# Kernel optimization log

Hardware: AMD Instinct MI355X
Metric: run time of the kernel (lower is better)

## Reference

```python
import jax, jax.numpy as jnp
import numpy as np
import math

B = 4096
D = 768
HID = 256
C_OLD = 100
C_NEW = 100
NUM_CLASSES = 200
EPSILON = 0.05
TAU = 0.1
EPS = 1e-8
NEG_INF = -1e9


def _l2_normalize(x):
    # matches F.normalize(p=2, dim=1, eps=1e-12)
    n = jnp.linalg.norm(x, axis=1, keepdims=True)
    return x / jnp.maximum(n, 1e-12)


def setup_inputs() -> dict:
    key = jax.random.key(0)
    k1, k2, k3, k4, k5, k6, k7 = jax.random.split(key, 7)
    z_u = jax.random.normal(k1, (B, D), dtype=jnp.float32)
    logits = jax.random.normal(k2, (B, NUM_CLASSES), dtype=jnp.float32)
    old_class_indices = jnp.arange(C_OLD, dtype=jnp.int64 if jax.config.jax_enable_x64 else jnp.int32)
    new_class_indices = jnp.arange(C_OLD, C_OLD + C_NEW, dtype=old_class_indices.dtype)
    base_features = jax.random.normal(k3, (B, D), dtype=jnp.float32)
    s = 1.0 / math.sqrt(D)
    f1_w = jax.random.uniform(k4, (HID, D), dtype=jnp.float32, minval=-s, maxval=s)
    f1_b = jax.random.uniform(k5, (HID,), dtype=jnp.float32, minval=-s, maxval=s)
    f2_w = jax.random.uniform(k6, (HID, D), dtype=jnp.float32, minval=-s, maxval=s)
    f2_b = jax.random.uniform(k7, (HID,), dtype=jnp.float32, minval=-s, maxval=s)
    return {"z_u": z_u, "logits": logits, "old_class_indices": old_class_indices,
            "new_class_indices": new_class_indices, "base_features": base_features,
            "f1_w": f1_w, "f1_b": f1_b, "f2_w": f2_w, "f2_b": f2_b}


def reference(z_u, logits, old_class_indices, new_class_indices, base_features,
              f1_w, f1_b, f2_w, f2_b):
    num_old = old_class_indices.shape[0]
    active = jnp.concatenate([old_class_indices, new_class_indices])

    # ---- soft entropy regularization ----
    probs = jax.nn.softmax(logits[:, active], axis=1)   # (B, C_old+C_new)
    mean_probs = probs.mean(axis=0)
    p_old = mean_probs[:num_old].sum()
    p_new = mean_probs[num_old:].sum()
    loss_inter = (p_old * jnp.log(p_old + EPS) + p_new * jnp.log(p_new + EPS)
                  + math.log(2.0))
    p_old_in = mean_probs[:num_old] / (p_old + EPS)
    loss_old_in = jnp.sum(p_old_in * jnp.log(p_old_in + EPS)) + math.log(num_old)
    p_new_in = mean_probs[num_old:] / (p_new + EPS)
    num_new = new_class_indices.shape[0]
    if num_new > 1:
        loss_new_in = jnp.sum(p_new_in * jnp.log(p_new_in + EPS)) + math.log(num_new)
    else:
        loss_new_in = jnp.float32(0.0)
    loss_entropy = loss_inter + loss_old_in + loss_new_in

    # ---- neighborhood mask from frozen base features ----
    base_norm = _l2_normalize(base_features)
    base_sim = base_norm @ base_norm.T                  # (B, B)
    eye = jnp.eye(base_sim.shape[0], dtype=bool)
    mask = (base_sim > EPSILON) & ~eye                  # (B, B) bool

    # ---- contrastive similarities ----
    z_norm = _l2_normalize(z_u)
    sim = z_norm @ z_norm.T                             # (B, B)

    f1_z = z_u @ f1_w.T + f1_b                          # (B, HID)
    f2_z = z_u @ f2_w.T + f2_b
    attn_logits = jnp.where(mask, f1_z @ f2_z.T, NEG_INF)
    w_ik = jax.nn.softmax(attn_logits, axis=1) * mask.astype(sim.dtype)

    exp_sim = jnp.where(eye, 0.0, jnp.exp(sim / TAU))
    denom = exp_sim.sum(axis=1, keepdims=True)
    log_prob = sim / TAU - jnp.log(denom + EPS)

    num_neighbors = mask.sum(axis=1).astype(sim.dtype)  # (B,)
    valid = num_neighbors > 0
    loss_i = -(w_ik * mask.astype(sim.dtype) * log_prob).sum(axis=1)
    per_sample = jnp.where(valid, loss_i / jnp.maximum(num_neighbors, 1.0), 0.0)
    n_valid = valid.sum().astype(sim.dtype)
    loss_contrastive = jnp.where(n_valid > 0,
                                 per_sample.sum() / jnp.maximum(n_valid, 1.0),
                                 0.0)

    total_loss = loss_entropy + loss_contrastive
    return total_loss
```

## Files before the change

### kernel.cpp

```cpp
#include <hip/hip_runtime.h>
#include <hip/hip_fp8.h>


#define B_N   4096
#define D_N   768
#define HID_N 256
#define NCLS  200

typedef __attribute__((ext_vector_type(8))) short v8s;
typedef __attribute__((ext_vector_type(4))) short v4ss;
typedef __attribute__((ext_vector_type(4))) float v4f;

__device__ __forceinline__ unsigned short f2bf(float x) {
    unsigned int u = __float_as_uint(x);
    unsigned int r = (u + 0x7FFFu + ((u >> 16) & 1u)) >> 16;
    return (unsigned short)r;
}
__device__ __forceinline__ float bf2f(unsigned short h) {
    return __uint_as_float((unsigned int)h << 16);
}
__device__ __forceinline__ unsigned char f2fp8(float x) {
    __hip_fp8_e4m3 v(x);
    return (unsigned char)v.__x;
}
__device__ __forceinline__ unsigned int pack4fp8(float a, float b, float c, float d) {
    return (unsigned int)f2fp8(a) | ((unsigned int)f2fp8(b) << 8) |
           ((unsigned int)f2fp8(c) << 16) | ((unsigned int)f2fp8(d) << 24);
}

__device__ __forceinline__ void gld16c(const unsigned char* g, unsigned char* l) {
    __builtin_amdgcn_global_load_lds(
        (__attribute__((address_space(1))) void*)g,
        (__attribute__((address_space(3))) void*)l, 16, 0, 0);
}

#define ZERO_ACC(a) { _Pragma("unroll") for (int _i = 0; _i < 4; _i++) \
    _Pragma("unroll") for (int _j = 0; _j < 4; _j++) a[_i][_j] = (v4f){0.f,0.f,0.f,0.f}; }

__global__ __launch_bounds__(256) void pre_all(
    const float* __restrict__ z, const float* __restrict__ base,
    const float* __restrict__ w1, const float* __restrict__ w2,
    const float* __restrict__ b1, const float* __restrict__ b2,
    const float* __restrict__ logits, const int* __restrict__ oldi,
    const int* __restrict__ newi,
    unsigned char* __restrict__ zn8, unsigned char* __restrict__ bn8,
    unsigned char* __restrict__ f1z8, unsigned char* __restrict__ f2z8,
    float* __restrict__ mpart, float* __restrict__ accums)
{
    __shared__ __align__(16) unsigned char shmem[2 * 64 * 72 * 2];
    int tid = threadIdx.x;

    if (blockIdx.x < 512) {
        unsigned short* Al = (unsigned short*)shmem;
        unsigned short* Bl = Al + 64 * 72;
        int f = blockIdx.x;
        int which = f >> 8;
        int t6 = f & 255;
        int mBase = (t6 >> 2) * 64;
        int nBase = (t6 & 3) * 64;
        const float* wsrc = which ? w2 : w1;
        const float* bias = which ? b2 : b1;
        unsigned char* outz = which ? f2z8 : f1z8;
        int lane = tid & 63, wave = tid >> 6, quad = lane >> 4, col = lane & 15;
        v4f acc[4];
        #pragma unroll
        for (int i = 0; i < 4; i++) acc[i] = (v4f){0.f, 0.f, 0.f, 0.f};
        for (int kc = 0; kc < D_N; kc += 64) {
            __syncthreads();
            #pragma unroll
            for (int s = 0; s < 4; s++) {
                int slot = s * 256 + tid;
                int row = slot >> 4, k4 = slot & 15;
                float4 va = *(const float4*)(z + (size_t)(mBase + row) * D_N + kc + k4 * 4);
                float4 vb = *(const float4*)(wsrc + (size_t)(nBase + row) * D_N + kc + k4 * 4);
                v4ss sa, sb;
                sa[0] = (short)f2bf(va.x); sa[1] = (short)f2bf(va.y);
                sa[2] = (short)f2bf(va.z); sa[3] = (short)f2bf(va.w);
                sb[0] = (short)f2bf(vb.x); sb[1] = (short)f2bf(vb.y);
                sb[2] = (short)f2bf(vb.z); sb[3] = (short)f2bf(vb.w);
                *(v4ss*)(Al + row * 72 + k4 * 4) = sa;
                *(v4ss*)(Bl + row * 72 + k4 * 4) = sb;
            }
            __syncthreads();
            #pragma unroll
            for (int kk = 0; kk < 2; kk++) {
                v8s af = *(const v8s*)(Al + (wave * 16 + col) * 72 + kk * 32 + quad * 8);
                #pragma unroll
                for (int tc = 0; tc < 4; tc++) {
                    v8s bf = *(const v8s*)(Bl + (tc * 16 + col) * 72 + kk * 32 + quad * 8);
                    acc[tc] = __builtin_amdgcn_mfma_f32_16x16x32_bf16(af, bf, acc[tc], 0, 0, 0);
                }
            }
        }
        #pragma unroll
        for (int tc = 0; tc < 4; tc++) {
            int gcol = nBase + tc * 16 + col;
            float bv = bias[gcol];
            #pragma unroll
            for (int reg = 0; reg < 4; reg++) {
                int grow = mBase + wave * 16 + quad * 4 + reg;
                int sw8 = ((grow >> 3) & 1) << 3;
                outz[(size_t)grow * HID_N + (gcol ^ sw8)] =
                    f2fp8(4.0f * (acc[tc][reg] + bv));
            }
        }
        return;
    }
    if (blockIdx.x < 768) {
        int* act = (int*)shmem;
        float* accs = (float*)(shmem + 1024);
        int sb = blockIdx.x - 512;
        int lane = tid & 63, wave = tid >> 6;
        if (sb == 0 && tid < 4) accums[tid] = 0.0f;
        if (tid < NCLS) act[tid] = (tid < 100) ? oldi[tid] : newi[tid - 100];
        accs[tid] = 0.f; accs[256 + tid] = 0.f; accs[512 + tid] = 0.f; accs[768 + tid] = 0.f;
        __syncthreads();
        int a0 = act[lane], a1 = act[lane + 64], a2 = act[lane + 128];
        int a3 = (lane < 8) ? act[lane + 192] : 0;
        int r0 = sb * 16 + wave * 4;
        float c0 = 0.f, c1 = 0.f, c2 = 0.f, c3 = 0.f;
        for (int i = 0; i < 4; i++) {
            const float* lr = logits + (size_t)(r0 + i) * NCLS;
            float x0 = lr[a0], x1 = lr[a1], x2 = lr[a2];
            float x3 = (lane < 8) ? lr[a3] : -3.0e38f;
            float m = fmaxf(fmaxf(x0, x1), fmaxf(x2, x3));
            #pragma unroll
            for (int s = 32; s > 0; s >>= 1) m = fmaxf(m, __shfl_xor(m, s));
            float e0 = __expf(x0 - m), e1 = __expf(x1 - m), e2 = __expf(x2 - m);
            float e3 = (lane < 8) ? __expf(x3 - m) : 0.f;
            float sm = e0 + e1 + e2 + e3;
            #pragma unroll
            for (int s = 32; s > 0; s >>= 1) sm += __shfl_xor(sm, s);
            float inv = 1.0f / sm;
            c0 += e0 * inv; c1 += e1 * inv; c2 += e2 * inv; c3 += e3 * inv;
        }
        accs[wave * 256 + lane] = c0; accs[wave * 256 + lane + 64] = c1;
        accs[wave * 256 + lane + 128] = c2;
        if (lane < 8) accs[wave * 256 + lane + 192] = c3;
        __syncthreads();
        mpart[(size_t)tid * 256 + sb] =
            accs[tid] + accs[256 + tid] + accs[512 + tid] + accs[768 + tid];
        return;
    }
    {
        int nb = blockIdx.x - 768;
        int lane = tid & 63, wave = tid >> 6;
        #pragma unroll
        for (int rr = 0; rr < 2; rr++) {
            int row = nb * 8 + rr * 4 + wave;
            const float* zr = z    + (size_t)row * D_N;
            const float* br = base + (size_t)row * D_N;
            float4 zv0 = *(const float4*)(zr + (size_t)lane * 4);
            float4 zv1 = *(const float4*)(zr + (size_t)(lane + 64) * 4);
            float4 zv2 = *(const float4*)(zr + (size_t)(lane + 128) * 4);
            float4 bv0 = *(const float4*)(br + (size_t)lane * 4);
            float4 bv1 = *(const float4*)(br + (size_t)(lane + 64) * 4);
            float4 bv2 = *(const float4*)(br + (size_t)(lane + 128) * 4);
            float s1 = zv0.x*zv0.x + zv0.y*zv0.y + zv0.z*zv0.z + zv0.w*zv0.w
                     + zv1.x*zv1.x + zv1.y*zv1.y + zv1.z*zv1.z + zv1.w*zv1.w
                     + zv2.x*zv2.x + zv2.y*zv2.y + zv2.z*zv2.z + zv2.w*zv2.w;
            float s2 = bv0.x*bv0.x + bv0.y*bv0.y + bv0.z*bv0.z + bv0.w*bv0.w
                     + bv1.x*bv1.x + bv1.y*bv1.y + bv1.z*bv1.z + bv1.w*bv1.w
                     + bv2.x*bv2.x + bv2.y*bv2.y + bv2.z*bv2.z + bv2.w*bv2.w;
            #pragma unroll
            for (int m = 32; m > 0; m >>= 1) {
                s1 += __shfl_xor(s1, m);
                s2 += __shfl_xor(s2, m);
            }
            float sc1 = 16.0f / fmaxf(sqrtf(s1), 1e-12f);
            float sc2 = 16.0f / fmaxf(sqrtf(s2), 1e-12f);
            size_t o = (size_t)row * D_N;
            int sw8 = ((row >> 3) & 1) << 3;
            *(unsigned int*)(zn8 + o + (((lane      ) * 4) ^ sw8)) =
                pack4fp8(zv0.x*sc1, zv0.y*sc1, zv0.z*sc1, zv0.w*sc1);
            *(unsigned int*)(zn8 + o + (((lane +  64) * 4) ^ sw8)) =
                pack4fp8(zv1.x*sc1, zv1.y*sc1, zv1.z*sc1, zv1.w*sc1);
            *(unsigned int*)(zn8 + o + (((lane + 128) * 4) ^ sw8)) =
                pack4fp8(zv2.x*sc1, zv2.y*sc1, zv2.z*sc1, zv2.w*sc1);
            *(unsigned int*)(bn8 + o + (((lane      ) * 4) ^ sw8)) =
                pack4fp8(bv0.x*sc2, bv0.y*sc2, bv0.z*sc2, bv0.w*sc2);
            *(unsigned int*)(bn8 + o + (((lane +  64) * 4) ^ sw8)) =
                pack4fp8(bv1.x*sc2, bv1.y*sc2, bv1.z*sc2, bv1.w*sc2);
            *(unsigned int*)(bn8 + o + (((lane + 128) * 4) ^ sw8)) =
                pack4fp8(bv2.x*sc2, bv2.y*sc2, bv2.z*sc2, bv2.w*sc2);
        }
    }
}

__global__ __launch_bounds__(256, 2) void main_fused(
    const unsigned char* __restrict__ zn8, const unsigned char* __restrict__ bn8,
    const unsigned char* __restrict__ f1z8, const unsigned char* __restrict__ f2z8,
    float* __restrict__ partials)
{
    __shared__ __align__(16) unsigned char S[4 * 128 * 128];
    unsigned char* S0 = S;
    unsigned char* S1 = S + 1 * 128 * 128;
    unsigned char* S2 = S + 2 * 128 * 128;
    unsigned char* S3 = S + 3 * 128 * 128;
    int tid = threadIdx.x, lane = tid & 63, wave = tid >> 6, quad = lane >> 4, col = lane & 15;
    int wr = wave >> 1, wc = wave & 1;
    int ib = blockIdx.x, jc = blockIdx.y;
    int rBase = ib * 128 + wr * 64;
    int cBase = jc * 128 + wc * 64;
    const int r8 = lane >> 3;
    const int kbl8 = (lane & 7) ^ r8;
    const int sub8 = ((quad & 1) ^ (col >> 3)) << 3;

    v4f accB[4][4], accS[4][4];
    ZERO_ACC(accB); ZERO_ACC(accS);
    for (int kc = 0; kc < D_N; kc += 128) {
        __syncthreads();
        #pragma unroll
        for (int s = 0; s < 4; s++) {
            int rowbase = s * 32 + wave * 8;
            size_t rOff = (size_t)(ib * 128 + rowbase + r8) * D_N + kc + kbl8 * 16;
            size_t cOff = (size_t)(jc * 128 + rowbase + r8) * D_N + kc + kbl8 * 16;
            gld16c(bn8 + rOff, S0 + rowbase * 128);
            gld16c(bn8 + cOff, S1 + rowbase * 128);
            gld16c(zn8 + rOff, S2 + rowbase * 128);
            gld16c(zn8 + cOff, S3 + rowbase * 128);
        }
        __syncthreads();
        #pragma unroll
        for (int kk = 0; kk < 4; kk++) {
            int gbase = kk * 2 + (quad >> 1);
            int off = ((gbase ^ (col & 7)) << 4) + sub8;
            long a1[4], b1[4], a2[4], b2[4];
            #pragma unroll
            for (int t = 0; t < 4; t++) {
                int rA = (wr * 64 + t * 16 + col) * 128;
                int rB = (wc * 64 + t * 16 + col) * 128;
                a1[t] = *(const long*)(S0 + rA + off);
                b1[t] = *(const long*)(S1 + rB + off);
                a2[t] = *(const long*)(S2 + rA + off);
                b2[t] = *(const long*)(S3 + rB + off);
            }
            #pragma unroll
            for (int tr = 0; tr < 4; tr++)
                #pragma unroll
                for (int tc = 0; tc < 4; tc++) {
                    accB[tr][tc] = __builtin_amdgcn_mfma_f32_16x16x32_fp8_fp8(
                        a1[tr], b1[tc], accB[tr][tc], 0, 0, 0);
                    accS[tr][tc] = __builtin_amdgcn_mfma_f32_16x16x32_fp8_fp8(
                        a2[tr], b2[tc], accS[tr][tc], 0, 0, 0);
                }
        }
    }

    unsigned char* F1 = S0;
    unsigned char* F2 = S0 + 32768;
    __syncthreads();
    {
        int r4 = lane >> 4;
        #pragma unroll
        for (int s = 0; s < 8; s++) {
            int rowbase = s * 16 + wave * 4;
            int row = rowbase + r4;
            int kb = (lane & 15) ^ (row & 15);
            gld16c(f1z8 + (size_t)(ib * 128 + row) * HID_N + kb * 16, F1 + rowbase * 256);
            gld16c(f2z8 + (size_t)(jc * 128 + row) * HID_N + kb * 16, F2 + rowbase * 256);
        }
    }

    unsigned long long mb = 0ull;
    #pragma unroll
    for (int tr = 0; tr < 4; tr++)
        #pragma unroll
        for (int tc = 0; tc < 4; tc++)
            #pragma unroll
            for (int reg = 0; reg < 4; reg++) {
                int grow = rBase + tr * 16 + quad * 4 + reg;
                int gcol = cBase + tc * 16 + col;
                if (accB[tr][tc][reg] > 12.8f && grow != gcol)
                    mb |= 1ull << (tr * 16 + tc * 4 + reg);
            }

    float dsum[16];
    #pragma unroll
    for (int i = 0; i < 16; i++) dsum[i] = 0.f;
    unsigned int svp[4][4][2];
    #pragma unroll
    for (int tr = 0; tr < 4; tr++)
        #pragma unroll
        for (int tc = 0; tc < 4; tc++) {
            float s0 = accS[tr][tc][0] * 0.00390625f;
            float s1 = accS[tr][tc][1] * 0.00390625f;
            float s2 = accS[tr][tc][2] * 0.00390625f;
            float s3 = accS[tr][tc][3] * 0.00390625f;
            float svv[4] = {s0, s1, s2, s3};
            #pragma unroll
            for (int reg = 0; reg < 4; reg++) {
                int grow = rBase + tr * 16 + quad * 4 + reg;
                int gcol = cBase + tc * 16 + col;
                if (grow != gcol) dsum[tr * 4 + reg] += __expf(svv[reg] * 10.0f);
            }
            svp[tr][tc][0] = ((unsigned int)f2bf(s1) << 16) | f2bf(s0);
            svp[tr][tc][1] = ((unsigned int)f2bf(s3) << 16) | f2bf(s2);
        }

    v4f accA[4][4]; ZERO_ACC(accA);
    __syncthreads();
    #pragma unroll
    for (int kk = 0; kk < 8; kk++) {
        int gbase = kk * 2 + (quad >> 1);
        int off = ((gbase ^ col) << 4) + sub8;
        long af[4], bf[4];
        #pragma unroll
        for (int t = 0; t < 4; t++) {
            af[t] = *(const long*)(F1 + (wr * 64 + t * 16 + col) * 256 + off);
            bf[t] = *(const long*)(F2 + (wc * 64 + t * 16 + col) * 256 + off);
        }
        #pragma unroll
        for (int tr = 0; tr < 4; tr++)
            #pragma unroll
            for (int tc = 0; tc < 4; tc++)
                accA[tr][tc] = __builtin_amdgcn_mfma_f32_16x16x32_fp8_fp8(
                    af[tr], bf[tc], accA[tr][tc], 0, 0, 0);
    }

    float lsum[16], asum[16], nnf[16];
    #pragma unroll
    for (int i = 0; i < 16; i++) { lsum[i] = 0.f; asum[i] = 0.f; nnf[i] = 0.f; }
    #pragma unroll
    for (int tr = 0; tr < 4; tr++)
        #pragma unroll
        for (int tc = 0; tc < 4; tc++)
            #pragma unroll
            for (int reg = 0; reg < 4; reg++) {
                if ((mb >> (tr * 16 + tc * 4 + reg)) & 1ull) {
                    int slot = tr * 4 + reg;
                    float e = __expf(accA[tr][tc][reg] * 0.0625f);
                    unsigned int pk = svp[tr][tc][reg >> 1];
                    float sv = bf2f((unsigned short)((reg & 1) ? (pk >> 16) : (pk & 0xFFFF)));
                    lsum[slot] += e;
                    asum[slot] += e * sv;
                    nnf[slot] += 1.f;
                }
            }

    #pragma unroll
    for (int i = 0; i < 16; i++) {
        #pragma unroll
        for (int m = 1; m < 16; m <<= 1) {
            lsum[i] += __shfl_xor(lsum[i], m);
            asum[i] += __shfl_xor(asum[i], m);
            dsum[i] += __shfl_xor(dsum[i], m);
            nnf[i]  += __shfl_xor(nnf[i], m);
        }
        if (col == 0) {
            int row = rBase + (i >> 2) * 16 + quad * 4 + (i & 3);
            float4 v; v.x = lsum[i]; v.y = asum[i]; v.z = dsum[i]; v.w = nnf[i];
            *(float4*)(partials + ((size_t)row * 64 + jc * 2 + wc) * 4) = v;
        }
    }
}

__global__ __launch_bounds__(256) void row_reduce_fin(
    const float* __restrict__ partials, const float* __restrict__ mpart,
    float* __restrict__ acc, float* __restrict__ out)
{
    int tid = threadIdx.x;
    int row = blockIdx.x * 64 + (tid >> 2);
    int sub = tid & 3;
    const float4* p = (const float4*)partials + (size_t)row * 64 + sub * 16;
    float L = 0.f, A = 0.f, Dn = 0.f, NN = 0.f;
    #pragma unroll
    for (int c = 0; c < 16; c++) { float4 v = p[c]; L += v.x; A += v.y; Dn += v.z; NN += v.w; }
    #pragma unroll
    for (int m = 1; m < 4; m <<= 1) {
        L += __shfl_xor(L, m); A += __shfl_xor(A, m);
        Dn += __shfl_xor(Dn, m); NN += __shfl_xor(NN, m);
    }
    float per = 0.f, val = 0.f;
    if (sub == 0 && NN > 0.5f) {
        per = (logf(Dn + 1e-8f) - 10.0f * (A / L)) / NN;
        val = 1.0f;
    }
    __shared__ float red[256];
    __shared__ float r2s[256];
    __shared__ int amLast;
    red[tid] = per; r2s[tid] = val; __syncthreads();
    for (int s = 128; s > 0; s >>= 1) {
        if (tid < s) { red[tid] += red[tid + s]; r2s[tid] += r2s[tid + s]; }
        __syncthreads();
    }
    if (tid == 0) {
        atomicAdd(&acc[0], red[0]);
        atomicAdd(&acc[1], r2s[0]);
        __threadfence();
        int old = atomicAdd((int*)&acc[2], 1);
        amLast = (old == (int)gridDim.x - 1);
    }
    __syncthreads();
    if (!amLast) return;

    __shared__ float bcast[2];
    float pcl = 0.0f;
    if (tid < NCLS) {
        const float4* mp = (const float4*)(mpart + (size_t)tid * 256);
        float s = 0.f;
        #pragma unroll
        for (int c = 0; c < 64; c++) { float4 v = mp[c]; s += v.x + v.y + v.z + v.w; }
        pcl = s * (1.0f / 4096.0f);
    }
    red[tid] = (tid < 100) ? pcl : 0.0f; __syncthreads();
    for (int s = 128; s > 0; s >>= 1) { if (tid < s) red[tid] += red[tid + s]; __syncthreads(); }
    if (tid == 0) bcast[0] = red[0];
    __syncthreads();
    red[tid] = (tid >= 100 && tid < NCLS) ? pcl : 0.0f; __syncthreads();
    for (int s = 128; s > 0; s >>= 1) { if (tid < s) red[tid] += red[tid + s]; __syncthreads(); }
    if (tid == 0) bcast[1] = red[0];
    __syncthreads();
    float p_old = bcast[0], p_new = bcast[1];

    float t = 0.0f;
    if (tid < 100)       { float q = pcl / (p_old + 1e-8f); t = q * logf(q + 1e-8f); }
    else if (tid < NCLS) { float q = pcl / (p_new + 1e-8f); t = q * logf(q + 1e-8f); }
    red[tid] = t; __syncthreads();
    for (int s = 128; s > 0; s >>= 1) { if (tid < s) red[tid] += red[tid + s]; __syncthreads(); }

    if (tid == 0) {
        float s0 = __hip_atomic_load(&acc[0], __ATOMIC_RELAXED, __HIP_MEMORY_SCOPE_AGENT);
        float s1 = __hip_atomic_load(&acc[1], __ATOMIC_RELAXED, __HIP_MEMORY_SCOPE_AGENT);
        float loss_inter = p_old * logf(p_old + 1e-8f) + p_new * logf(p_new + 1e-8f)
                           + 0.69314718056f;
        float loss_entropy = loss_inter + red[0] + 2.0f * 4.60517018599f;
        float lc = (s1 > 0.5f) ? s0 / s1 : 0.0f;
        out[0] = loss_entropy + lc;
    }
}

extern "C" void kernel_launch(void* const* d_in, const int* in_sizes, int n_in,
                              void* d_out, int out_size, void* d_ws, size_t ws_size,
                              hipStream_t stream)
{
    const float* z_u    = (const float*)d_in[0];
    const float* logits = (const float*)d_in[1];
    const int*   oldi   = (const int*)d_in[2];
    const int*   newi   = (const int*)d_in[3];
    const float* basef  = (const float*)d_in[4];
    const float* f1w    = (const float*)d_in[5];
    const float* f1b    = (const float*)d_in[6];
    const float* f2w    = (const float*)d_in[7];
    const float* f2b    = (const float*)d_in[8];
    float* out = (float*)d_out;

    unsigned char* zn8   = (unsigned char*)d_ws;
    unsigned char* bn8   = zn8 + (size_t)B_N * D_N;
    unsigned char* f1z8  = bn8 + (size_t)B_N * D_N;
    unsigned char* f2z8  = f1z8 + (size_t)B_N * HID_N;
    float* partials = (float*)(f2z8 + (size_t)B_N * HID_N);
    float* mpart    = partials + (size_t)B_N * 64 * 4;
    float* accums   = mpart + 256 * 256;

    pre_all<<<512 + 256 + 512, 256, 0, stream>>>(
        z_u, basef, f1w, f2w, f1b, f2b, logits, oldi, newi,
        zn8, bn8, f1z8, f2z8, mpart, accums);
    main_fused<<<dim3(32, 32), 256, 0, stream>>>(zn8, bn8, f1z8, f2z8, partials);
    row_reduce_fin<<<64, 256, 0, stream>>>(partials, mpart, accums, out);
}
```

Measured before the change: 169.5 us.

## Exploit symmetry of similarity matrices with a persistent triangular-tile job scheduler

The base and z similarity GEMMs are symmetric, so only upper-triangular 128x128 tile pairs (split into 64-row halves) and diagonal tiles are computed. Each tile's results are reduced for both the row block and the transposed column block. The f1·f2ᵀ attention product is not symmetric, so it is computed in both orientations. Work is handed out by a persistent 512-block kernel that pulls jobs from an atomic counter, which is reset in the preprocessing kernel. This roughly halves the K=768 MFMA work and its loads, at the cost of atomics, extra per-job synchronisation and a more complex epilogue.

```diff
diff --git a/kernel.cpp b/kernel.cpp
--- a/kernel.cpp
+++ b/kernel.cpp
@@ -6,6 +6,7 @@
 #define D_N   768
 #define HID_N 256
 #define NCLS  200
+#define NJOBS 1056u
 
 typedef __attribute__((ext_vector_type(8))) short v8s;
 typedef __attribute__((ext_vector_type(4))) short v4ss;
@@ -16,9 +17,6 @@
     unsigned int r = (u + 0x7FFFu + ((u >> 16) & 1u)) >> 16;
     return (unsigned short)r;
 }
-__device__ __forceinline__ float bf2f(unsigned short h) {
-    return __uint_as_float((unsigned int)h << 16);
-}
 __device__ __forceinline__ unsigned char f2fp8(float x) {
     __hip_fp8_e4m3 v(x);
     return (unsigned char)v.__x;
@@ -34,7 +32,7 @@
         (__attribute__((address_space(3))) void*)l, 16, 0, 0);
 }
 
-#define ZERO_ACC(a) { _Pragma("unroll") for (int _i = 0; _i < 4; _i++) \
+#define ZERO_ACC24(a) { _Pragma("unroll") for (int _i = 0; _i < 2; _i++) \
     _Pragma("unroll") for (int _j = 0; _j < 4; _j++) a[_i][_j] = (v4f){0.f,0.f,0.f,0.f}; }
 
 __global__ __launch_bounds__(256) void pre_all(
@@ -111,7 +109,7 @@
         float* accs = (float*)(shmem + 1024);
         int sb = blockIdx.x - 512;
         int lane = tid & 63, wave = tid >> 6;
-        if (sb == 0 && tid < 4) accums[tid] = 0.0f;
+        if (sb == 0 && tid < 6) accums[tid] = 0.0f;
         if (tid < NCLS) act[tid] = (tid < 100) ? oldi[tid] : newi[tid - 100];
         accs[tid] = 0.f; accs[256 + tid] = 0.f; accs[512 + tid] = 0.f; accs[768 + tid] = 0.f;
         __syncthreads();
@@ -190,167 +188,259 @@
 __global__ __launch_bounds__(256, 2) void main_fused(
     const unsigned char* __restrict__ zn8, const unsigned char* __restrict__ bn8,
     const unsigned char* __restrict__ f1z8, const unsigned char* __restrict__ f2z8,
-    float* __restrict__ partials)
+    float* __restrict__ partials, int* __restrict__ jobcnt)
 {
-    __shared__ __align__(16) unsigned char S[4 * 128 * 128];
-    unsigned char* S0 = S;
-    unsigned char* S1 = S + 1 * 128 * 128;
-    unsigned char* S2 = S + 2 * 128 * 128;
-    unsigned char* S3 = S + 3 * 128 * 128;
-    int tid = threadIdx.x, lane = tid & 63, wave = tid >> 6, quad = lane >> 4, col = lane & 15;
-    int wr = wave >> 1, wc = wave & 1;
-    int ib = blockIdx.x, jc = blockIdx.y;
-    int rBase = ib * 128 + wr * 64;
-    int cBase = jc * 128 + wc * 64;
+    __shared__ __align__(16) unsigned char S[53248];
+    __shared__ int sh_j;
+    unsigned char* SA_B = S;
+    unsigned char* SA_S = S + 8192;
+    unsigned char* SB_B = S + 16384;
+    unsigned char* SB_S = S + 32768;
+    unsigned char* F1   = S;
+    unsigned char* F2   = S + 16384;
+    float4* red = (float4*)(S + 49152);
+
+    int tid = threadIdx.x, lane = tid & 63, wave = tid >> 6;
+    int quad = lane >> 4, col = lane & 15;
+    int wr3 = wave >> 1, wc3 = wave & 1;
     const int r8 = lane >> 3;
     const int kbl8 = (lane & 7) ^ r8;
     const int sub8 = ((quad & 1) ^ (col >> 3)) << 3;
 
-    v4f accB[4][4], accS[4][4];
-    ZERO_ACC(accB); ZERO_ACC(accS);
-    for (int kc = 0; kc < D_N; kc += 128) {
-        __syncthreads();
-        #pragma unroll
-        for (int s = 0; s < 4; s++) {
-            int rowbase = s * 32 + wave * 8;
-            size_t rOff = (size_t)(ib * 128 + rowbase + r8) * D_N + kc + kbl8 * 16;
-            size_t cOff = (size_t)(jc * 128 + rowbase + r8) * D_N + kc + kbl8 * 16;
-            gld16c(bn8 + rOff, S0 + rowbase * 128);
-            gld16c(bn8 + cOff, S1 + rowbase * 128);
-            gld16c(zn8 + rOff, S2 + rowbase * 128);
-            gld16c(zn8 + cOff, S3 + rowbase * 128);
-        }
-        __syncthreads();
-        #pragma unroll
-        for (int kk = 0; kk < 4; kk++) {
+    for (;;) {
+        __syncthreads();
+        if (tid == 0) sh_j = atomicAdd(jobcnt, 1);
+        __syncthreads();
+        unsigned int j = (unsigned int)sh_j;
+        if (j >= NJOBS) return;
+
+        int ib, jc, h; bool diag;
+        if (j < 992u) {
+            int pp = (int)(j >> 1); h = (int)(j & 1u); diag = false;
+            int t = (int)((1.0f + sqrtf(8.0f * (float)pp + 1.0f)) * 0.5f);
+            t = (t < 1) ? 1 : ((t > 31) ? 31 : t);
+            while (t > 1  && t * (t - 1) / 2 > pp) --t;
+            while (t < 31 && (t + 1) * t / 2 <= pp) ++t;
+            jc = t; ib = pp - t * (t - 1) / 2;
+        } else {
+            int dd = (int)(j - 992u); ib = jc = dd >> 1; h = dd & 1; diag = true;
+        }
+        int aRow0 = ib * 128 + h * 64;
+        int bRow0 = jc * 128;
+
+        v4f accB[2][4], accS[2][4];
+        ZERO_ACC24(accB); ZERO_ACC24(accS);
+        for (int kc = 0; kc < D_N; kc += 128) {
+            __syncthreads();
+            #pragma unroll
+            for (int s = 0; s < 4; s++) {
+                int rowbase = s * 32 + wave * 8;
+                size_t gOff = (size_t)(bRow0 + rowbase + r8) * D_N + kc + kbl8 * 16;
+                gld16c(bn8 + gOff, SB_B + rowbase * 128);
+                gld16c(zn8 + gOff, SB_S + rowbase * 128);
+            }
+            if (!diag) {
+                #pragma unroll
+                for (int s = 0; s < 2; s++) {
+                    int rowbase = s * 32 + wave * 8;
+                    size_t gOff = (size_t)(aRow0 + rowbase + r8) * D_N + kc + kbl8 * 16;
+                    gld16c(bn8 + gOff, SA_B + rowbase * 128);
+                    gld16c(zn8 + gOff, SA_S + rowbase * 128);
+                }
+            }
+            __syncthreads();
+            const unsigned char* AB = diag ? (SB_B + h * 64 * 128) : SA_B;
+            const unsigned char* AS = diag ? (SB_S + h * 64 * 128) : SA_S;
+            #pragma unroll
+            for (int kk = 0; kk < 4; kk++) {
+                int gbase = kk * 2 + (quad >> 1);
+                int off = ((gbase ^ (col & 7)) << 4) + sub8;
+                long a1[2], a2[2], b1[4], b2[4];
+                #pragma unroll
+                for (int t = 0; t < 2; t++) {
+                    int rA = (wr3 * 32 + t * 16 + col) * 128;
+                    a1[t] = *(const long*)(AB + rA + off);
+                    a2[t] = *(const long*)(AS + rA + off);
+                }
+                #pragma unroll
+                for (int t = 0; t < 4; t++) {
+                    int rB = (wc3 * 64 + t * 16 + col) * 128;
+                    b1[t] = *(const long*)(SB_B + rB + off);
+                    b2[t] = *(const long*)(SB_S + rB + off);
+                }
+                #pragma unroll
+                for (int tr = 0; tr < 2; tr++)
+                    #pragma unroll
+                    for (int tc = 0; tc < 4; tc++) {
+                        accB[tr][tc] = __builtin_amdgcn_mfma_f32_16x16x32_fp8_fp8(
+                            a1[tr], b1[tc], accB[tr][tc], 0, 0, 0);
+                        accS[tr][tc] = __builtin_amdgcn_mfma_f32_16x16x32_fp8_fp8(
+                            a2[tr], b2[tc], accS[tr][tc], 0, 0, 0);
+                    }
+            }
+        }
+
+        __syncthreads();
+        {
+            int r4 = lane >> 4;
+            #pragma unroll
+            for (int s = 0; s < 8; s++) {
+                int rowbase = s * 16 + wave * 4;
+                int row = rowbase + r4;
+                int kb = (lane & 15) ^ (row & 15);
+                gld16c(f2z8 + (size_t)(bRow0 + row) * HID_N + kb * 16, F2 + rowbase * 256);
+            }
+            #pragma unroll
+            for (int s = 0; s < 4; s++) {
+                int rowbase = s * 16 + wave * 4;
+                int row = rowbase + r4;
+                int kb = (lane & 15) ^ (row & 15);
+                gld16c(f1z8 + (size_t)(aRow0 + row) * HID_N + kb * 16, F1 + rowbase * 256);
+            }
+        }
+
+        unsigned int mb = 0u;
+        #pragma unroll
+        for (int tr = 0; tr < 2; tr++)
+            #pragma unroll
+            for (int tc = 0; tc < 4; tc++)
+                #pragma unroll
+                for (int reg = 0; reg < 4; reg++) {
+                    int grow = aRow0 + wr3 * 32 + tr * 16 + quad * 4 + reg;
+                    int gcol = bRow0 + wc3 * 64 + tc * 16 + col;
+                    if (accB[tr][tc][reg] > 12.8f && grow != gcol)
+                        mb |= 1u << (tr * 16 + tc * 4 + reg);
+                }
+
+        v4f accA[2][4]; ZERO_ACC24(accA);
+        __syncthreads();
+        #pragma unroll
+        for (int kk = 0; kk < 8; kk++) {
             int gbase = kk * 2 + (quad >> 1);
-            int off = ((gbase ^ (col & 7)) << 4) + sub8;
-            long a1[4], b1[4], a2[4], b2[4];
-            #pragma unroll
-            for (int t = 0; t < 4; t++) {
-                int rA = (wr * 64 + t * 16 + col) * 128;
-                int rB = (wc * 64 + t * 16 + col) * 128;
-                a1[t] = *(const long*)(S0 + rA + off);
-                b1[t] = *(const long*)(S1 + rB + off);
-                a2[t] = *(const long*)(S2 + rA + off);
-                b2[t] = *(const long*)(S3 + rB + off);
-            }
-            #pragma unroll
-            for (int tr = 0; tr < 4; tr++)
-                #pragma unroll
-                for (int tc = 0; tc < 4; tc++) {
-                    accB[tr][tc] = __builtin_amdgcn_mfma_f32_16x16x32_fp8_fp8(
-                        a1[tr], b1[tc], accB[tr][tc], 0, 0, 0);
-                    accS[tr][tc] = __builtin_amdgcn_mfma_f32_16x16x32_fp8_fp8(
-                        a2[tr], b2[tc], accS[tr][tc], 0, 0, 0);
-                }
-        }
-    }
-
-    unsigned char* F1 = S0;
-    unsigned char* F2 = S0 + 32768;
-    __syncthreads();
-    {
-        int r4 = lane >> 4;
-        #pragma unroll
-        for (int s = 0; s < 8; s++) {
-            int rowbase = s * 16 + wave * 4;
-            int row = rowbase + r4;
-            int kb = (lane & 15) ^ (row & 15);
-            gld16c(f1z8 + (size_t)(ib * 128 + row) * HID_N + kb * 16, F1 + rowbase * 256);
-            gld16c(f2z8 + (size_t)(jc * 128 + row) * HID_N + kb * 16, F2 + rowbase * 256);
-        }
-    }
-
-    unsigned long long mb = 0ull;
-    #pragma unroll
-    for (int tr = 0; tr < 4; tr++)
-        #pragma unroll
-        for (int tc = 0; tc < 4; tc++)
-            #pragma unroll
-            for (int reg = 0; reg < 4; reg++) {
-                int grow = rBase + tr * 16 + quad * 4 + reg;
-                int gcol = cBase + tc * 16 + col;
-                if (accB[tr][tc][reg] > 12.8f && grow != gcol)
-                    mb |= 1ull << (tr * 16 + tc * 4 + reg);
-            }
-
-    float dsum[16];
-    #pragma unroll
-    for (int i = 0; i < 16; i++) dsum[i] = 0.f;
-    unsigned int svp[4][4][2];
-    #pragma unroll
-    for (int tr = 0; tr < 4; tr++)
-        #pragma unroll
-        for (int tc = 0; tc < 4; tc++) {
-            float s0 = accS[tr][tc][0] * 0.00390625f;
-            float s1 = accS[tr][tc][1] * 0.00390625f;
-            float s2 = accS[tr][tc][2] * 0.00390625f;
-            float s3 = accS[tr][tc][3] * 0.00390625f;
-            float svv[4] = {s0, s1, s2, s3};
-            #pragma unroll
-            for (int reg = 0; reg < 4; reg++) {
-                int grow = rBase + tr * 16 + quad * 4 + reg;
-                int gcol = cBase + tc * 16 + col;
-                if (grow != gcol) dsum[tr * 4 + reg] += __expf(svv[reg] * 10.0f);
-            }
-            svp[tr][tc][0] = ((unsigned int)f2bf(s1) << 16) | f2bf(s0);
-            svp[tr][tc][1] = ((unsigned int)f2bf(s3) << 16) | f2bf(s2);
-        }
-
-    v4f accA[4][4]; ZERO_ACC(accA);
-    __syncthreads();
-    #pragma unroll
-    for (int kk = 0; kk < 8; kk++) {
-        int gbase = kk * 2 + (quad >> 1);
-        int off = ((gbase ^ col) << 4) + sub8;
-        long af[4], bf[4];
-        #pragma unroll
-        for (int t = 0; t < 4; t++) {
-            af[t] = *(const long*)(F1 + (wr * 64 + t * 16 + col) * 256 + off);
-            bf[t] = *(const long*)(F2 + (wc * 64 + t * 16 + col) * 256 + off);
-        }
-        #pragma unroll
-        for (int tr = 0; tr < 4; tr++)
+            int off = ((gbase ^ col) << 4) + sub8;
+            long af[2], bf[4];
+            #pragma unroll
+            for (int t = 0; t < 2; t++)
+                af[t] = *(const long*)(F1 + (wr3 * 32 + t * 16 + col) * 256 + off);
+            #pragma unroll
+            for (int t = 0; t < 4; t++)
+                bf[t] = *(const long*)(F2 + (wc3 * 64 + t * 16 + col) * 256 + off);
+            #pragma unroll
+            for (int tr = 0; tr < 2; tr++)
+                #pragma unroll
+                for (int tc = 0; tc < 4; tc++)
+                    accA[tr][tc] = __builtin_amdgcn_mfma_f32_16x16x32_fp8_fp8(
+                        af[tr], bf[tc], accA[tr][tc], 0, 0, 0);
+        }
+
+        __syncthreads();
+        if (!diag) {
+            int r4 = lane >> 4;
+            #pragma unroll
+            for (int s = 0; s < 8; s++) {
+                int rowbase = s * 16 + wave * 4;
+                int row = rowbase + r4;
+                int kb = (lane & 15) ^ (row & 15);
+                gld16c(f1z8 + (size_t)(bRow0 + row) * HID_N + kb * 16, F2 + rowbase * 256);
+            }
+            #pragma unroll
+            for (int s = 0; s < 4; s++) {
+                int rowbase = s * 16 + wave * 4;
+                int row = rowbase + r4;
+                int kb = (lane & 15) ^ (row & 15);
+                gld16c(f2z8 + (size_t)(aRow0 + row) * HID_N + kb * 16, F1 + rowbase * 256);
+            }
+        }
+
+        #pragma unroll
+        for (int tr = 0; tr < 2; tr++) {
+            float ls[4], as[4], nn[4], ds[4];
+            #pragma unroll
+            for (int r = 0; r < 4; r++) { ls[r]=0.f; as[r]=0.f; nn[r]=0.f; ds[r]=0.f; }
             #pragma unroll
             for (int tc = 0; tc < 4; tc++)
-                accA[tr][tc] = __builtin_amdgcn_mfma_f32_16x16x32_fp8_fp8(
-                    af[tr], bf[tc], accA[tr][tc], 0, 0, 0);
-    }
-
-    float lsum[16], asum[16], nnf[16];
-    #pragma unroll
-    for (int i = 0; i < 16; i++) { lsum[i] = 0.f; asum[i] = 0.f; nnf[i] = 0.f; }
-    #pragma unroll
-    for (int tr = 0; tr < 4; tr++)
-        #pragma unroll
-        for (int tc = 0; tc < 4; tc++)
-            #pragma unroll
-            for (int reg = 0; reg < 4; reg++) {
-                if ((mb >> (tr * 16 + tc * 4 + reg)) & 1ull) {
-                    int slot = tr * 4 + reg;
-                    float e = __expf(accA[tr][tc][reg] * 0.0625f);
-                    unsigned int pk = svp[tr][tc][reg >> 1];
-                    float sv = bf2f((unsigned short)((reg & 1) ? (pk >> 16) : (pk & 0xFFFF)));
-                    lsum[slot] += e;
-                    asum[slot] += e * sv;
-                    nnf[slot] += 1.f;
-                }
-            }
-
-    #pragma unroll
-    for (int i = 0; i < 16; i++) {
-        #pragma unroll
-        for (int m = 1; m < 16; m <<= 1) {
-            lsum[i] += __shfl_xor(lsum[i], m);
-            asum[i] += __shfl_xor(asum[i], m);
-            dsum[i] += __shfl_xor(dsum[i], m);
-            nnf[i]  += __shfl_xor(nnf[i], m);
-        }
-        if (col == 0) {
-            int row = rBase + (i >> 2) * 16 + quad * 4 + (i & 3);
-            float4 v; v.x = lsum[i]; v.y = asum[i]; v.z = dsum[i]; v.w = nnf[i];
-            *(float4*)(partials + ((size_t)row * 64 + jc * 2 + wc) * 4) = v;
+                #pragma unroll
+                for (int reg = 0; reg < 4; reg++) {
+                    float sv = accS[tr][tc][reg] * 0.00390625f;
+                    int grow = aRow0 + wr3 * 32 + tr * 16 + quad * 4 + reg;
+                    int gcol = bRow0 + wc3 * 64 + tc * 16 + col;
+                    if (grow != gcol) ds[reg] += __expf(sv * 10.0f);
+                    if ((mb >> (tr * 16 + tc * 4 + reg)) & 1u) {
+                        float e = __expf(accA[tr][tc][reg] * 0.0625f);
+                        ls[reg] += e; as[reg] += e * sv; nn[reg] += 1.f;
+                    }
+                }
+            #pragma unroll
+            for (int r = 0; r < 4; r++) {
+                #pragma unroll
+                for (int m = 1; m < 16; m <<= 1) {
+                    ls[r] += __shfl_xor(ls[r], m);
+                    as[r] += __shfl_xor(as[r], m);
+                    ds[r] += __shfl_xor(ds[r], m);
+                    nn[r] += __shfl_xor(nn[r], m);
+                }
+                if (col == 0) {
+                    int row = aRow0 + wr3 * 32 + tr * 16 + quad * 4 + r;
+                    float4 v; v.x = ls[r]; v.y = as[r]; v.z = ds[r]; v.w = nn[r];
+                    *(float4*)(partials + ((size_t)row * 64 + jc * 2 + wc3) * 4) = v;
+                }
+            }
+        }
+
+        if (!diag) {
+            ZERO_ACC24(accA);
+            __syncthreads();
+            #pragma unroll
+            for (int kk = 0; kk < 8; kk++) {
+                int gbase = kk * 2 + (quad >> 1);
+                int off = ((gbase ^ col) << 4) + sub8;
+                long af[2], bf[4];
+                #pragma unroll
+                for (int t = 0; t < 2; t++)
+                    af[t] = *(const long*)(F1 + (wr3 * 32 + t * 16 + col) * 256 + off);
+                #pragma unroll
+                for (int t = 0; t < 4; t++)
+                    bf[t] = *(const long*)(F2 + (wc3 * 64 + t * 16 + col) * 256 + off);
+                #pragma unroll
+                for (int tr = 0; tr < 2; tr++)
+                    #pragma unroll
+                    for (int tc = 0; tc < 4; tc++)
+                        accA[tr][tc] = __builtin_amdgcn_mfma_f32_16x16x32_fp8_fp8(
+                            af[tr], bf[tc], accA[tr][tc], 0, 0, 0);
+            }
+            #pragma unroll
+            for (int tc = 0; tc < 4; tc++) {
+                float l2 = 0.f, a2 = 0.f, d2 = 0.f, n2 = 0.f;
+                #pragma unroll
+                for (int tr = 0; tr < 2; tr++)
+                    #pragma unroll
+                    for (int reg = 0; reg < 4; reg++) {
+                        float sv = accS[tr][tc][reg] * 0.00390625f;
+                        d2 += __expf(sv * 10.0f);
+                        if ((mb >> (tr * 16 + tc * 4 + reg)) & 1u) {
+                            float e = __expf(accA[tr][tc][reg] * 0.0625f);
+                            l2 += e; a2 += e * sv; n2 += 1.f;
+                        }
+                    }
+                #pragma unroll
+                for (int m = 16; m < 64; m <<= 1) {
+                    l2 += __shfl_xor(l2, m);
+                    a2 += __shfl_xor(a2, m);
+                    d2 += __shfl_xor(d2, m);
+                    n2 += __shfl_xor(n2, m);
+                }
+                if (lane < 16) {
+                    float4 v; v.x = l2; v.y = a2; v.z = d2; v.w = n2;
+                    red[wr3 * 128 + wc3 * 64 + tc * 16 + lane] = v;
+                }
+            }
+            __syncthreads();
+            if (tid < 128) {
+                float4 u = red[tid], v = red[128 + tid];
+                float4 w; w.x = u.x + v.x; w.y = u.y + v.y;
+                w.z = u.z + v.z; w.w = u.w + v.w;
+                *(float4*)(partials + ((size_t)(bRow0 + tid) * 64 + ib * 2 + h) * 4) = w;
+            }
         }
     }
 }
@@ -452,10 +542,11 @@
     float* partials = (float*)(f2z8 + (size_t)B_N * HID_N);
     float* mpart    = partials + (size_t)B_N * 64 * 4;
     float* accums   = mpart + 256 * 256;
+    int*   jobcnt   = (int*)(accums + 4);
 
     pre_all<<<512 + 256 + 512, 256, 0, stream>>>(
         z_u, basef, f1w, f2w, f1b, f2b, logits, oldi, newi,
         zn8, bn8, f1z8, f2z8, mpart, accums);
-    main_fused<<<dim3(32, 32), 256, 0, stream>>>(zn8, bn8, f1z8, f2z8, partials);
+    main_fused<<<512, 256, 0, stream>>>(zn8, bn8, f1z8, f2z8, partials, jobcnt);
     row_reduce_fin<<<64, 256, 0, stream>>>(partials, mpart, accums, out);
 }
```

Measured after the change: 168.7 us. No clear change (-0.5%).
